# Optimization experiments

Measured on AMD Instinct MI355X. Metric: run time of the kernel, lower is better.

Reference implementation:

```python
import jax, jax.numpy as jnp
import numpy as np
from jax import lax

N = 100000   # input points
M = 100000   # output points
CIN = 64
COUT = 64
K = 3        # cubic kernel size
G = 50       # grid side (points live at voxel centers of a G^3 grid)
SHIFT = 1    # coordinate shift so border queries (coord -1) stay non-negative
B = 64       # per-axis encode base, > G + K; key fits easily in int32


def _encode(c):
    # c: [..., 3] int32 xyz voxel coords -> unique int32 key
    c = c + SHIFT
    return (c[..., 2] * B + c[..., 1]) * B + c[..., 0]


def setup_inputs() -> dict:
    rng = np.random.RandomState(0)
    total = G ** 3

    def decode(idx):
        x = idx % G
        y = (idx // G) % G
        z = idx // (G * G)
        # +0.5 moves points to voxel centers (as in the layer's docstring example)
        return np.stack([x, y, z], axis=1).astype(np.float32) + 0.5

    inp_positions = jnp.asarray(decode(rng.permutation(total)[:N]))
    out_positions = jnp.asarray(decode(rng.permutation(total)[:M]))

    key = jax.random.key(0)
    k1, k2 = jax.random.split(key, 2)
    inp_features = jax.random.normal(k1, (N, CIN), jnp.float32)
    kernel = jax.random.normal(k2, (K, K, K, CIN, COUT), jnp.float32) * 0.05
    bias = jnp.zeros((COUT,), jnp.float32)
    voxel_size = jnp.ones((), jnp.float32)
    return {
        "inp_features": inp_features,
        "inp_positions": inp_positions,
        "out_positions": out_positions,
        "voxel_size": voxel_size,
        "kernel": kernel,
        "bias": bias,
    }


def reference(inp_features, inp_positions, out_positions, voxel_size, kernel, bias):
    # SparseConv on a regular grid: odd cubic kernel -> offset = 0, Linf radius
    # K*voxel*0.51 selects exactly the K^3 voxel neighborhood. Nearest-neighbor
    # interpolation with identity mapping maps relative offset d in [-r, r]^3
    # to filter tap index d + r on each axis (x = width = last spatial dim).
    inp_coord = jnp.floor(inp_positions / voxel_size).astype(jnp.int32)  # [N,3]
    out_coord = jnp.floor(out_positions / voxel_size).astype(jnp.int32)  # [M,3]

    # sorted-key hash table over input voxels
    keys = _encode(inp_coord)                    # [N]
    order = jnp.argsort(keys)
    skeys = keys[order]
    feats = inp_features[order]                  # [N, Cin]

    r = K // 2
    K3 = K ** 3
    ks = jnp.arange(K3)
    # flat kernel order is (z, y, x) to match kernel.reshape(K3, Cin, Cout)
    d_xyz = jnp.stack([ks % K - r, (ks // K) % K - r, ks // (K * K) - r],
                      axis=1).astype(jnp.int32)  # [K3, 3]
    Kmat = kernel.reshape(K3, CIN, COUT)

    n_inp = skeys.shape[0]

    def step(acc, xs):
        d, W = xs                                 # d: [3], W: [Cin, Cout]
        qk = _encode(out_coord + d)               # [M]
        p = jnp.searchsorted(skeys, qk)
        pc = jnp.clip(p, 0, n_inp - 1)
        found = (skeys[pc] == qk)[:, None]        # [M, 1]
        g = jnp.where(found, feats[pc], 0.0)      # [M, Cin]
        return acc + g @ W, None

    out0 = jnp.zeros((out_coord.shape[0], COUT), inp_features.dtype)
    out, _ = lax.scan(step, out0, (d_xyz, Kmat))
    return out + bias
```

## Files before the change

kernel.cpp:

```cpp
#include <hip/hip_runtime.h>
#include <math.h>

#define GY 54
#define ZD 58
#define NROWS (ZD*GY*64)

#define HX 10
#define HY 6
#define HXY 60
#define NH 600
#define NBX 7
#define NBY 13
#define NBZ 7
#define NBRICK (NBX*NBY*NBZ)
#define SLAB 80

typedef __bf16  bf16x8 __attribute__((ext_vector_type(8)));
typedef float  f32x16 __attribute__((ext_vector_type(16)));

__global__ void prep_kernel(const float* __restrict__ ipos, int n,
                            const float* __restrict__ opos, int m,
                            const float* __restrict__ vsp,
                            const float* __restrict__ W,
                            int* __restrict__ imap, int* __restrict__ ikey,
                            int* __restrict__ omap, int* __restrict__ okey,
                            __bf16* __restrict__ Wt4) {
    int i = blockIdx.x * 256 + threadIdx.x;
    float vs = vsp[0];
    if (i < n) {
        int x = (int)floorf(ipos[3*i+0] / vs) + 1;
        int y = (int)floorf(ipos[3*i+1] / vs) + 1;
        int z = (int)floorf(ipos[3*i+2] / vs) + 1;
        int key = (z * GY + y) * 64 + x;
        ikey[i] = key;
        imap[key] = i;
    } else if (i < n + m) {
        int j = i - n;
        int x = (int)floorf(opos[3*j+0] / vs) + 1;
        int y = (int)floorf(opos[3*j+1] / vs) + 1;
        int z = (int)floorf(opos[3*j+2] / vs) + 1;
        int key = (z * GY + y) * 64 + x;
        okey[j] = key;
        omap[key] = j;
    } else if (i < n + m + 27*64*64) {
        int k  = i - n - m;
        int t  = k >> 12;
        int r  = k & 4095;
        int ci = r >> 6;
        int co = r & 63;
        int p   = ci >> 4;
        int cil = ci & 15;
        Wt4[(((p * 27 + t) << 6) + co) * 16 + cil] = (__bf16)W[k];
    }
}

__global__ __launch_bounds__(256, 2) void conv_kernel(
    const float* __restrict__ feats,
    const __bf16* __restrict__ Wt4,
    const float* __restrict__ bias,
    const int*   __restrict__ imap,
    const int*   __restrict__ ikey,
    const int*   __restrict__ omap,
    const int*   __restrict__ okey,
    float*       __restrict__ out,
    int N, int M)
{
    __shared__ __align__(16) __bf16 halo[NH * 16];
    __shared__ __align__(16) __bf16 Bq[27 * 64 * 16];
    __shared__ int ridx[NH];
    __shared__ int obuf[256];

    const int tid = threadIdx.x;

    int q = (blockIdx.x & 7) * SLAB + (blockIdx.x >> 3);
    if (q >= NBRICK) return;
    const int bx = q % NBX;
    int rem = q / NBX;
    const int by = rem % NBY;
    const int bz = rem / NBY;

    #pragma unroll
    for (int it = 0; it < 3; ++it) {
        int r = it * 256 + tid;
        if (r < NH) {
            int xs = r % HX;
            int t2 = r / HX;
            int ys = t2 % HY;
            int zs = t2 / HY;
            int key = ((bz*8 + zs) * GY + (by*4 + ys)) * 64 + (bx*8 + xs);
            int idx = imap[key];
            int c = min(max(idx, 0), N - 1);
            ridx[r] = (idx >= 0 && idx < N && ikey[c] == key) ? idx : -1;
        }
    }
    {
        int x = tid & 7, y = (tid >> 3) & 3, z = tid >> 5;
        int key = ((bz*8 + z + 1) * GY + (by*4 + y + 1)) * 64 + (bx*8 + x + 1);
        int o = omap[key];
        int c = min(max(o, 0), M - 1);
        obuf[tid] = (o >= 0 && o < M && okey[c] == key) ? o : -1;
    }

    const int wave  = tid >> 6;
    const int lane  = tid & 63;
    const int lrow  = lane & 31;
    const int halfk = lane >> 5;
    const int xv = lrow & 7, yv = (lrow >> 3) & 3;
    const int arow0 = (2*wave + 1) * HXY + (yv + 1) * HX + (xv + 1);
    const __bf16* Ab0 = halo + arow0 * 16 + halfk * 8;
    const __bf16* Ab1 = Ab0 + HXY * 16;
    const __bf16* Bb0 = Bq + lrow * 16 + halfk * 8;
    const __bf16* Bb1 = Bb0 + 32 * 16;

    f32x16 acc00, acc01, acc10, acc11;
    #pragma unroll
    for (int i = 0; i < 16; ++i) { acc00[i]=0.f; acc01[i]=0.f; acc10[i]=0.f; acc11[i]=0.f; }

    __syncthreads();

    #pragma unroll 1
    for (int p = 0; p < 4; ++p) {
        if (p) __syncthreads();

        #pragma unroll
        for (int it = 0; it < 5; ++it) {
            int task = it * 256 + tid;
            if (task < NH * 2) {
                int r = task >> 1, hf = task & 1;
                int idx = ridx[r];
                bf16x8 v;
                if (idx >= 0) {
                    const float4* s = (const float4*)(feats + (size_t)idx * 64 + p * 16 + hf * 8);
                    float4 f0 = s[0], f1 = s[1];
                    v[0]=(__bf16)f0.x; v[1]=(__bf16)f0.y; v[2]=(__bf16)f0.z; v[3]=(__bf16)f0.w;
                    v[4]=(__bf16)f1.x; v[5]=(__bf16)f1.y; v[6]=(__bf16)f1.z; v[7]=(__bf16)f1.w;
                } else {
                    #pragma unroll
                    for (int j = 0; j < 8; ++j) v[j] = (__bf16)0.f;
                }
                *(bf16x8*)(halo + r * 16 + hf * 8) = v;
            }
        }

        {
            const __bf16* Wp = Wt4 + (size_t)p * 27648;
            #pragma unroll
            for (int it = 0; it < 14; ++it) {
                int task = it * 256 + tid;
                if (task < 3456) {
                    *(bf16x8*)(Bq + task * 8) = *(const bf16x8*)(Wp + task * 8);
                }
            }
        }

        __syncthreads();

        #pragma unroll
        for (int t = 0; t < 27; ++t) {
            const int dx = t % 3 - 1;
            const int dy = (t / 3) % 3 - 1;
            const int dz = t / 9 - 1;
            const int doff = (dz * HXY + dy * HX + dx) * 16;

            bf16x8 a0 = *(const bf16x8*)(Ab0 + doff);
            bf16x8 a1 = *(const bf16x8*)(Ab1 + doff);
            bf16x8 b0 = *(const bf16x8*)(Bb0 + t * 1024);
            bf16x8 b1 = *(const bf16x8*)(Bb1 + t * 1024);

            acc00 = __builtin_amdgcn_mfma_f32_32x32x16_bf16(a0, b0, acc00, 0, 0, 0);
            acc01 = __builtin_amdgcn_mfma_f32_32x32x16_bf16(a0, b1, acc01, 0, 0, 0);
            acc10 = __builtin_amdgcn_mfma_f32_32x32x16_bf16(a1, b0, acc10, 0, 0, 0);
            acc11 = __builtin_amdgcn_mfma_f32_32x32x16_bf16(a1, b1, acc11, 0, 0, 0);
        }
    }

    const int col0 = lrow, col1 = 32 + lrow;
    const float bv0 = bias[col0], bv1 = bias[col1];
    #pragma unroll
    for (int r = 0; r < 16; ++r) {
        int mrow = (r & 3) + 8 * (r >> 2) + 4 * halfk;
        int o0 = obuf[(2*wave)     * 32 + mrow];
        int o1 = obuf[(2*wave + 1) * 32 + mrow];
        if (o0 >= 0) {
            out[(size_t)o0 * 64 + col0] = acc00[r] + bv0;
            out[(size_t)o0 * 64 + col1] = acc01[r] + bv1;
        }
        if (o1 >= 0) {
            out[(size_t)o1 * 64 + col0] = acc10[r] + bv0;
            out[(size_t)o1 * 64 + col1] = acc11[r] + bv1;
        }
    }
}

extern "C" void kernel_launch(void* const* d_in, const int* in_sizes, int n_in,
                              void* d_out, int out_size, void* d_ws, size_t ws_size,
                              hipStream_t stream) {
    const float* feats = (const float*)d_in[0];
    const float* ipos  = (const float*)d_in[1];
    const float* opos  = (const float*)d_in[2];
    const float* vsp   = (const float*)d_in[3];
    const float* W     = (const float*)d_in[4];
    const float* bias  = (const float*)d_in[5];

    int N = in_sizes[0] / 64;
    int M = out_size / 64;

    int*    imap = (int*)d_ws;
    int*    omap = imap + NROWS;
    int*    ikey = omap + NROWS;
    int*    okey = ikey + N;
    __bf16* Wt4  = (__bf16*)(okey + M);

    int total = N + M + 27*64*64;
    prep_kernel<<<(total + 255) / 256, 256, 0, stream>>>(ipos, N, opos, M, vsp, W,
                                                         imap, ikey, omap, okey, Wt4);
    conv_kernel<<<8 * SLAB, 256, 0, stream>>>(feats, Wt4, bias, imap, ikey, omap, okey,
                                              (float*)d_out, N, M);
}
```

Before: 146.0 us.

## Split weight staging into two tap chunks and swizzle LDS to cut bank conflicts

The 27-tap weight slice in shared memory is replaced by a 14-tap buffer that is loaded twice per channel chunk (taps 0-13, then 14-26). This roughly halves that LDS footprint so launch bounds can request three blocks per CU instead of two. Both the halo and weight layouts get an XOR swizzle of the 8-element halves, based on the row index, to reduce LDS bank conflicts on the MFMA operand loads. The cost is two extra block-wide barriers and an extra weight reload per channel chunk, and the higher occupancy target may squeeze registers.

```diff
diff --git a/kernel.cpp b/kernel.cpp
--- a/kernel.cpp
+++ b/kernel.cpp
@@ -14,6 +14,9 @@
 #define NBZ 7
 #define NBRICK (NBX*NBY*NBZ)
 #define SLAB 80
+
+#define TAPS_C0 14
+#define TAPS_C1 13
 
 typedef __bf16  bf16x8 __attribute__((ext_vector_type(8)));
 typedef float  f32x16 __attribute__((ext_vector_type(16)));
@@ -50,11 +53,14 @@
         int co = r & 63;
         int p   = ci >> 4;
         int cil = ci & 15;
-        Wt4[(((p * 27 + t) << 6) + co) * 16 + cil] = (__bf16)W[k];
+        int h   = cil >> 3;
+        int j   = cil & 7;
+        int g   = ((p * 27 + t) << 7) + (co << 1) + (h ^ ((co >> 2) & 1));
+        Wt4[(g << 3) + j] = (__bf16)W[k];
     }
 }
 
-__global__ __launch_bounds__(256, 2) void conv_kernel(
+__global__ __launch_bounds__(256, 3) void conv_kernel(
     const float* __restrict__ feats,
     const __bf16* __restrict__ Wt4,
     const float* __restrict__ bias,
@@ -66,7 +72,7 @@
     int N, int M)
 {
     __shared__ __align__(16) __bf16 halo[NH * 16];
-    __shared__ __align__(16) __bf16 Bq[27 * 64 * 16];
+    __shared__ __align__(16) __bf16 Bq[TAPS_C0 * 64 * 16];
     __shared__ int ridx[NH];
     __shared__ int obuf[256];
 
@@ -107,14 +113,29 @@
     const int halfk = lane >> 5;
     const int xv = lrow & 7, yv = (lrow >> 3) & 3;
     const int arow0 = (2*wave + 1) * HXY + (yv + 1) * HX + (xv + 1);
-    const __bf16* Ab0 = halo + arow0 * 16 + halfk * 8;
-    const __bf16* Ab1 = Ab0 + HXY * 16;
-    const __bf16* Bb0 = Bq + lrow * 16 + halfk * 8;
-    const __bf16* Bb1 = Bb0 + 32 * 16;
+    const __bf16* Bb0 = Bq + (((lrow << 1) + (halfk ^ ((lrow >> 2) & 1))) << 3);
+    const __bf16* Bb1 = Bb0 + 512;
 
     f32x16 acc00, acc01, acc10, acc11;
     #pragma unroll
     for (int i = 0; i < 16; ++i) { acc00[i]=0.f; acc01[i]=0.f; acc10[i]=0.f; acc11[i]=0.f; }
+
+    auto tap_body = [&](int t, int tc) {
+        const int dx = t % 3 - 1;
+        const int dy = (t / 3) % 3 - 1;
+        const int dz = t / 9 - 1;
+        const int drow = dz * HXY + dy * HX + dx;
+        int ar0 = arow0 + drow;
+        int sw0 = halfk ^ ((ar0 >> 2) & 1);
+        bf16x8 a0 = *(const bf16x8*)(halo + ar0 * 16 + (sw0 << 3));
+        bf16x8 a1 = *(const bf16x8*)(halo + (ar0 + HXY) * 16 + ((sw0 ^ 1) << 3));
+        bf16x8 b0 = *(const bf16x8*)(Bb0 + tc * 1024);
+        bf16x8 b1 = *(const bf16x8*)(Bb1 + tc * 1024);
+        acc00 = __builtin_amdgcn_mfma_f32_32x32x16_bf16(a0, b0, acc00, 0, 0, 0);
+        acc01 = __builtin_amdgcn_mfma_f32_32x32x16_bf16(a0, b1, acc01, 0, 0, 0);
+        acc10 = __builtin_amdgcn_mfma_f32_32x32x16_bf16(a1, b0, acc10, 0, 0, 0);
+        acc11 = __builtin_amdgcn_mfma_f32_32x32x16_bf16(a1, b1, acc11, 0, 0, 0);
+    };
 
     __syncthreads();
 
@@ -138,40 +159,41 @@
                     #pragma unroll
                     for (int j = 0; j < 8; ++j) v[j] = (__bf16)0.f;
                 }
-                *(bf16x8*)(halo + r * 16 + hf * 8) = v;
+                int sw = hf ^ ((r >> 2) & 1);
+                *(bf16x8*)(halo + r * 16 + (sw << 3)) = v;
             }
         }
 
         {
             const __bf16* Wp = Wt4 + (size_t)p * 27648;
             #pragma unroll
-            for (int it = 0; it < 14; ++it) {
+            for (int it = 0; it < 7; ++it) {
                 int task = it * 256 + tid;
-                if (task < 3456) {
+                *(bf16x8*)(Bq + task * 8) = *(const bf16x8*)(Wp + task * 8);
+            }
+        }
+
+        __syncthreads();
+
+        #pragma unroll
+        for (int t = 0; t < TAPS_C0; ++t) tap_body(t, t);
+
+        __syncthreads();
+
+        {
+            const __bf16* Wp = Wt4 + (size_t)p * 27648 + TAPS_C0 * 1024;
+            #pragma unroll
+            for (int it = 0; it < 7; ++it) {
+                int task = it * 256 + tid;
+                if (task < TAPS_C1 * 128)
                     *(bf16x8*)(Bq + task * 8) = *(const bf16x8*)(Wp + task * 8);
-                }
             }
         }
 
         __syncthreads();
 
         #pragma unroll
-        for (int t = 0; t < 27; ++t) {
-            const int dx = t % 3 - 1;
-            const int dy = (t / 3) % 3 - 1;
-            const int dz = t / 9 - 1;
-            const int doff = (dz * HXY + dy * HX + dx) * 16;
-
-            bf16x8 a0 = *(const bf16x8*)(Ab0 + doff);
-            bf16x8 a1 = *(const bf16x8*)(Ab1 + doff);
-            bf16x8 b0 = *(const bf16x8*)(Bb0 + t * 1024);
-            bf16x8 b1 = *(const bf16x8*)(Bb1 + t * 1024);
-
-            acc00 = __builtin_amdgcn_mfma_f32_32x32x16_bf16(a0, b0, acc00, 0, 0, 0);
-            acc01 = __builtin_amdgcn_mfma_f32_32x32x16_bf16(a0, b1, acc01, 0, 0, 0);
-            acc10 = __builtin_amdgcn_mfma_f32_32x32x16_bf16(a1, b0, acc10, 0, 0, 0);
-            acc11 = __builtin_amdgcn_mfma_f32_32x32x16_bf16(a1, b1, acc11, 0, 0, 0);
-        }
+        for (int t = TAPS_C0; t < 27; ++t) tap_body(t, t - TAPS_C0);
     }
 
     const int col0 = lrow, col1 = 32 + lrow;
```

New measurement: 253.7 us. +73.8%, slower.
